# Kernel tuning notes

Hardware: AMD Instinct MI355X
Metric: run time of the kernel (lower is better)

The kernel has to match this reference:

```python
import jax, jax.numpy as jnp
import numpy as np

B, S, HID = 1, 2048, 4096
NH, NKV, D = 32, 8, 128          # query heads, kv heads, head_dim
GROUPS = NH // NKV               # GQA repeat factor = 4
WINDOW = 1024                    # sliding-window size
ROPE_BASE = 10000.0


def setup_inputs() -> dict:
    key = jax.random.key(0)
    k = jax.random.split(key, 5)
    hidden_states = jax.random.normal(k[0], (B, S, HID), jnp.float32)
    Wq = jax.random.normal(k[1], (HID, HID), jnp.float32) * 0.02
    Wk = jax.random.normal(k[2], (NKV * D, HID), jnp.float32) * 0.02
    Wv = jax.random.normal(k[3], (NKV * D, HID), jnp.float32) * 0.02
    Wo = jax.random.normal(k[4], (HID, HID), jnp.float32) * 0.02
    position_ids = jnp.arange(S, dtype=jnp.int64 if jax.config.jax_enable_x64 else jnp.int32)[None, :]
    # Sliding-window causal additive mask [B,1,S,S]: key j visible to query i iff i-WINDOW < j <= i
    i = jnp.arange(S)
    visible = (i[None, :] <= i[:, None]) & (i[:, None] - i[None, :] < WINDOW)
    neg = jnp.finfo(jnp.float32).min
    attention_mask = jnp.where(visible, 0.0, neg)[None, None, :, :].astype(jnp.float32)
    return {"hidden_states": hidden_states, "attention_mask": attention_mask,
            "position_ids": position_ids, "Wq": Wq, "Wk": Wk, "Wv": Wv, "Wo": Wo}


def _rotate_half(x):
    x1, x2 = x[..., : D // 2], x[..., D // 2:]
    return jnp.concatenate((-x2, x1), axis=-1)


def _rope_cos_sin(position_ids, dtype):
    # inv_freq over even dims; gather-by-position_ids == direct indexing
    inv_freq = 1.0 / (ROPE_BASE ** (jnp.arange(0, D, 2, dtype=jnp.float32) / D))  # [D/2]
    freqs = position_ids.astype(jnp.float32)[..., None] * inv_freq                # [B,S,D/2]
    emb = jnp.concatenate((freqs, freqs), axis=-1)                                # [B,S,D]
    cos = jnp.cos(emb)[:, None, :, :].astype(dtype)                               # [B,1,S,D]
    sin = jnp.sin(emb)[:, None, :, :].astype(dtype)
    return cos, sin


def reference(hidden_states, attention_mask, position_ids, Wq, Wk, Wv, Wo):
    bsz, q_len, _ = hidden_states.shape
    # projections (nn.Linear: y = x @ W.T)
    q = (hidden_states @ Wq.T).reshape(bsz, q_len, NH, D).transpose(0, 2, 1, 3)    # [B,NH,S,D]
    k = (hidden_states @ Wk.T).reshape(bsz, q_len, NKV, D).transpose(0, 2, 1, 3)   # [B,NKV,S,D]
    v = (hidden_states @ Wv.T).reshape(bsz, q_len, NKV, D).transpose(0, 2, 1, 3)
    cos, sin = _rope_cos_sin(position_ids, q.dtype)
    q = q * cos + _rotate_half(q) * sin
    k = k * cos + _rotate_half(k) * sin
    # GQA repeat_kv (repeat_interleave along head dim)
    k = jnp.repeat(k, GROUPS, axis=1)                                              # [B,NH,S,D]
    v = jnp.repeat(v, GROUPS, axis=1)
    scores = jnp.einsum('bhqd,bhkd->bhqk', q, k) / np.sqrt(D)                       # [B,NH,S,S]
    scores = scores + attention_mask
    scores = jnp.maximum(scores, jnp.finfo(scores.dtype).min)
    probs = jax.nn.softmax(scores.astype(jnp.float32), axis=-1).astype(q.dtype)
    out = jnp.einsum('bhqk,bhkd->bhqd', probs, v)                                   # [B,NH,S,D]
    out = out.transpose(0, 2, 1, 3).reshape(bsz, q_len, HID)
    return out @ Wo.T
```

## Files before the change

kernel.cpp:

```cpp
#include <hip/hip_runtime.h>

#define S_LEN 2048
#define HID   4096
#define NH    32
#define NKV   8
#define DH    128
#define KVD   (NKV*DH)
#define WIN   1024
#define NTOT  6144

typedef __bf16 bf16_t;
typedef __bf16 bfrag  __attribute__((ext_vector_type(8)));
typedef __bf16 bf4    __attribute__((ext_vector_type(4)));
typedef float  ffrag  __attribute__((ext_vector_type(4)));
typedef float  facc   __attribute__((ext_vector_type(16)));

__global__ __launch_bounds__(256) void cvt4_kernel(const float* __restrict__ h,
    const float* __restrict__ Wq, const float* __restrict__ Wk, const float* __restrict__ Wv,
    bf16_t* __restrict__ hB, bf16_t* __restrict__ WqB,
    bf16_t* __restrict__ WkB, bf16_t* __restrict__ WvB) {
  int i = blockIdx.x * 256 + threadIdx.x;
  const int N0 = S_LEN * HID / 4;
  const int N1 = N0 + HID * HID / 4;
  const int N2 = N1 + KVD * HID / 4;
  const float* s; bf16_t* d; int off;
  if (i < N0)      { s = h;  d = hB;  off = i; }
  else if (i < N1) { s = Wq; d = WqB; off = i - N0; }
  else if (i < N2) { s = Wk; d = WkB; off = i - N1; }
  else             { s = Wv; d = WvB; off = i - N2; }
  ffrag v = *(const ffrag*)(s + (size_t)off * 4);
  bf4 o;
  o[0] = (bf16_t)v[0]; o[1] = (bf16_t)v[1]; o[2] = (bf16_t)v[2]; o[3] = (bf16_t)v[3];
  *(bf4*)(d + (size_t)off * 4) = o;
}

__global__ __launch_bounds__(256) void rope_table_kernel(float2* __restrict__ tab) {
  int i = blockIdx.x * 256 + threadIdx.x;
  int s = i >> 6, d = i & 63;
  float inv = exp2f((float)d * (-13.287712379549449f / 64.f));
  float ang = (float)s * inv;
  tab[i] = make_float2(cosf(ang), sinf(ang));
}

__device__ __forceinline__ void load_lds16(const bf16_t* g, bf16_t* l) {
  __builtin_amdgcn_global_load_lds((__attribute__((address_space(1))) void*)g,
                                   (__attribute__((address_space(3))) void*)l,
                                   16, 0, 0);
}

#define BARW() asm volatile("s_barrier" ::: "memory")
#define WAITV(n) asm volatile("s_waitcnt vmcnt(" #n ")" ::: "memory")
#define LGKM0() do { asm volatile("s_waitcnt lgkmcnt(0)" ::: "memory"); \
                     __builtin_amdgcn_sched_barrier(0); } while (0)

__device__ __forceinline__ bfrag cvt8(const float4& a, const float4& b) {
  bfrag w;
  w[0] = (bf16_t)a.x; w[1] = (bf16_t)a.y; w[2] = (bf16_t)a.z; w[3] = (bf16_t)a.w;
  w[4] = (bf16_t)b.x; w[5] = (bf16_t)b.y; w[6] = (bf16_t)b.z; w[7] = (bf16_t)b.w;
  return w;
}

__global__ __launch_bounds__(512, 4) void gemm_qkv_kernel(const bf16_t* __restrict__ hB,
                                                          const bf16_t* __restrict__ Wqkv,
                                                          bf16_t* __restrict__ C) {
  constexpr int K     = 4096;
  constexpr int NT    = K / 64;
  constexpr int ABUFE = 128 * 64;
  constexpr int BBUFE = 192 * 64;
  __shared__ __align__(16) bf16_t lds[2 * ABUFE + 2 * BBUFE];
  bf16_t* As0 = lds;
  bf16_t* Bs0 = lds + 2 * ABUFE;

  const int raw  = blockIdx.x;
  const int xcd  = raw & 7;
  const int slot = raw >> 3;
  const int bx   = xcd * 4 + (slot & 3);
  const int by   = slot >> 2;
  const int row0 = by * 128;
  const int col0 = bx * 192;

  const int tid  = threadIdx.x;
  const int wave = tid >> 6;
  const int lane = tid & 63;
  const int wr = wave >> 2, wc = wave & 3;
  const int n = lane & 15, qd = lane >> 4;

  const int rsub = tid >> 3;
  const int sg   = (tid & 7) ^ (rsub & 7);
  const bf16_t* Ag = hB   + (size_t)(row0 + rsub) * K + sg * 8;
  const bf16_t* Bg = Wqkv + (size_t)(col0 + rsub) * K + sg * 8;
  const int wbase = wave * 512;

  const int pg0 = ( qd      ^ (n & 7)) * 8;
  const int pg1 = ((4 | qd) ^ (n & 7)) * 8;
  const int abase = (wr * 64 + n) * 64;
  const int bbase = (wc * 48 + n) * 64;

  ffrag acc[4][3];
#pragma unroll
  for (int mt = 0; mt < 4; ++mt)
#pragma unroll
    for (int nt = 0; nt < 3; ++nt) {
      acc[mt][nt][0] = 0.f; acc[mt][nt][1] = 0.f; acc[mt][nt][2] = 0.f; acc[mt][nt][3] = 0.f;
    }

  auto STAGE = [&](int t, int s) {
    const int ko = t * 64;
    bf16_t* as = As0 + s * ABUFE + wbase;
    bf16_t* bs = Bs0 + s * BBUFE + wbase;
    load_lds16(Ag + ko, as);
    load_lds16(Ag + (size_t)64 * K + ko, as + 4096);
    load_lds16(Bg + ko, bs);
    load_lds16(Bg + (size_t)64 * K + ko, bs + 4096);
    load_lds16(Bg + (size_t)128 * K + ko, bs + 8192);
  };

  STAGE(0, 0); STAGE(1, 1);
  WAITV(5);
  BARW();

  for (int t = 0; t < NT; ++t) {
    const int s = t & 1;
    const bf16_t* Asl = As0 + s * ABUFE;
    const bf16_t* Bsl = Bs0 + s * BBUFE;
    bfrag av[4], bv[3];

#pragma unroll
    for (int mt = 0; mt < 4; ++mt) av[mt] = *(const bfrag*)(Asl + abase + mt * 1024 + pg0);
#pragma unroll
    for (int nt = 0; nt < 3; ++nt) bv[nt] = *(const bfrag*)(Bsl + bbase + nt * 1024 + pg0);
    __builtin_amdgcn_s_setprio(1);
#pragma unroll
    for (int mt = 0; mt < 4; ++mt)
#pragma unroll
      for (int nt = 0; nt < 3; ++nt)
        acc[mt][nt] = __builtin_amdgcn_mfma_f32_16x16x32_bf16(av[mt], bv[nt], acc[mt][nt], 0, 0, 0);
    __builtin_amdgcn_s_setprio(0);

#pragma unroll
    for (int mt = 0; mt < 4; ++mt) av[mt] = *(const bfrag*)(Asl + abase + mt * 1024 + pg1);
#pragma unroll
    for (int nt = 0; nt < 3; ++nt) bv[nt] = *(const bfrag*)(Bsl + bbase + nt * 1024 + pg1);
    __builtin_amdgcn_s_setprio(1);
#pragma unroll
    for (int mt = 0; mt < 4; ++mt)
#pragma unroll
      for (int nt = 0; nt < 3; ++nt)
        acc[mt][nt] = __builtin_amdgcn_mfma_f32_16x16x32_bf16(av[mt], bv[nt], acc[mt][nt], 0, 0, 0);
    __builtin_amdgcn_s_setprio(0);

    LGKM0();
    BARW();
    if (t + 2 < NT) STAGE(t + 2, s);
    if (t + 1 < NT) {
      if (t + 2 < NT) { WAITV(5); } else { WAITV(0); }
      BARW();
    }
  }

  const int orow = row0 + wr * 64 + qd * 4;
  const int ocol = col0 + wc * 48 + n;
#pragma unroll
  for (int mt = 0; mt < 4; ++mt)
#pragma unroll
    for (int nt = 0; nt < 3; ++nt)
#pragma unroll
      for (int r = 0; r < 4; ++r)
        C[(size_t)(orow + mt * 16 + r) * NTOT + (ocol + nt * 16)] = (bf16_t)acc[mt][nt][r];
}

__global__ __launch_bounds__(256, 2) void gemm_out_kernel(const bf16_t* __restrict__ A,
                                                          const float* __restrict__ Wo,
                                                          float* __restrict__ out) {
  constexpr int K     = 4096;
  constexpr int NT    = K / 64;
  constexpr int ABUFE = 128 * 64;
  constexpr int BBUFE = 128 * 64;
  __shared__ __align__(16) bf16_t lds[2 * ABUFE + 2 * BBUFE];
  bf16_t* As0 = lds;
  bf16_t* Bs0 = lds + 2 * ABUFE;

  const int raw  = blockIdx.x;
  const int xcd  = raw & 7;
  const int slot = raw >> 3;
  const int bx   = xcd * 4 + (slot & 3);
  const int by   = slot >> 2;
  const int row0 = by * 128;
  const int col0 = bx * 128;

  const int tid  = threadIdx.x;
  const int wave = tid >> 6;
  const int lane = tid & 63;
  const int wm = wave >> 1, wn = wave & 1;
  const int l31 = lane & 31, hi = lane >> 5, l7 = lane & 7;

  const int rsub = tid >> 3;
  const int gA   = (tid & 7) ^ (rsub & 7);
  const bf16_t* Ag = A + (size_t)(row0 + rsub) * K + gA * 8;
  const int wbase = wave * 512;

  const int gB = tid & 7;
  const float* Bgf = Wo + (size_t)(col0 + rsub) * K;
  const int bwoff = rsub * 64 + ((gB ^ (rsub & 7)) * 8);

  int pgk[4];
#pragma unroll
  for (int ks = 0; ks < 4; ++ks) pgk[ks] = ((ks * 2 + hi) ^ l7) * 8;
  const int aoff = (wm * 64 + l31) * 64;
  const int boff = (wn * 64 + l31) * 64;

  facc acc[2][2];
#pragma unroll
  for (int mt = 0; mt < 2; ++mt)
#pragma unroll
    for (int nt = 0; nt < 2; ++nt)
#pragma unroll
      for (int j = 0; j < 16; ++j) acc[mt][nt][j] = 0.f;

  float4 bb00, bb01, bb10, bb11, bb20, bb21, bb30, bb31;

#define OUT_LOADB(t) do { const int ko_ = (t) * 64 + gB * 8;                        \
    bb00 = *(const float4*)(Bgf + ko_);                                             \
    bb01 = *(const float4*)(Bgf + ko_ + 4);                                         \
    bb10 = *(const float4*)(Bgf + (size_t)32 * K + ko_);                            \
    bb11 = *(const float4*)(Bgf + (size_t)32 * K + ko_ + 4);                        \
    bb20 = *(const float4*)(Bgf + (size_t)64 * K + ko_);                            \
    bb21 = *(const float4*)(Bgf + (size_t)64 * K + ko_ + 4);                        \
    bb30 = *(const float4*)(Bgf + (size_t)96 * K + ko_);                            \
    bb31 = *(const float4*)(Bgf + (size_t)96 * K + ko_ + 4); } while (0)
#define OUT_WRITEB(s) do { bf16_t* bs_ = Bs0 + (s) * BBUFE;                         \
    *(bfrag*)&bs_[bwoff]        = cvt8(bb00, bb01);                                 \
    *(bfrag*)&bs_[2048 + bwoff] = cvt8(bb10, bb11);                                 \
    *(bfrag*)&bs_[4096 + bwoff] = cvt8(bb20, bb21);                                 \
    *(bfrag*)&bs_[6144 + bwoff] = cvt8(bb30, bb31); } while (0)

  auto STAGE_A = [&](int t, int s) {
    const int ko = t * 64;
    bf16_t* as = As0 + s * ABUFE + wbase;
#pragma unroll
    for (int i = 0; i < 4; ++i)
      load_lds16(Ag + (size_t)(i * 32) * K + ko, as + i * 2048);
  };

  STAGE_A(0, 0); OUT_LOADB(0);
  WAITV(0);
  OUT_WRITEB(0);
  STAGE_A(1, 1); OUT_LOADB(1);
  LGKM0();
  BARW();

  for (int t = 0; t < NT; ++t) {
    const int s = t & 1;
    const bf16_t* Asl = As0 + s * ABUFE;
    const bf16_t* Bsl = Bs0 + s * BBUFE;

#pragma unroll
    for (int ks = 0; ks < 4; ++ks) {
      bfrag av0 = *(const bfrag*)(Asl + aoff + pgk[ks]);
      bfrag av1 = *(const bfrag*)(Asl + aoff + 2048 + pgk[ks]);
      bfrag bv0 = *(const bfrag*)(Bsl + boff + pgk[ks]);
      bfrag bv1 = *(const bfrag*)(Bsl + boff + 2048 + pgk[ks]);
      __builtin_amdgcn_s_setprio(1);
      acc[0][0] = __builtin_amdgcn_mfma_f32_32x32x16_bf16(av0, bv0, acc[0][0], 0, 0, 0);
      acc[0][1] = __builtin_amdgcn_mfma_f32_32x32x16_bf16(av0, bv1, acc[0][1], 0, 0, 0);
      acc[1][0] = __builtin_amdgcn_mfma_f32_32x32x16_bf16(av1, bv0, acc[1][0], 0, 0, 0);
      acc[1][1] = __builtin_amdgcn_mfma_f32_32x32x16_bf16(av1, bv1, acc[1][1], 0, 0, 0);
      __builtin_amdgcn_s_setprio(0);
    }

    LGKM0();
    BARW();
    if (t + 2 < NT) STAGE_A(t + 2, s);
    if (t + 1 < NT) {
      if (t + 2 < NT) { WAITV(4); } else { WAITV(0); }
      OUT_WRITEB(s ^ 1);
      if (t + 2 < NT) OUT_LOADB(t + 2);
      LGKM0();
      BARW();
    }
  }

  const int orow = row0 + wm * 64 + 4 * hi;
  const int ocol = col0 + wn * 64 + l31;
#pragma unroll
  for (int mt = 0; mt < 2; ++mt)
#pragma unroll
    for (int nt = 0; nt < 2; ++nt)
#pragma unroll
      for (int j = 0; j < 16; ++j) {
        int r = orow + mt * 32 + (j & 3) + 8 * (j >> 2);
        out[(size_t)r * HID + (ocol + nt * 32)] = acc[mt][nt][j];
      }
#undef OUT_LOADB
#undef OUT_WRITEB
}

__global__ __launch_bounds__(256) void ropecvt_kernel(const bf16_t* __restrict__ Cqkv,
                                                      const float2* __restrict__ tab,
                                                      bf16_t* __restrict__ Qb,
                                                      bf16_t* __restrict__ Kb,
                                                      bf16_t* __restrict__ Vb) {
  int idx = blockIdx.x * 256 + threadIdx.x;
  int g  = idx & 7;
  int t  = idx >> 3;
  int hh = t % 48;
  int s  = t / 48;
  const bf16_t* r0 = Cqkv + (size_t)s * NTOT + hh * 128;
  bfrag a0 = *(const bfrag*)&r0[g * 8];
  bfrag a1 = *(const bfrag*)&r0[g * 8 + 64];
  bf16_t* p;
  bool rope;
  if (hh < NH)           { p = Qb + (size_t)s * HID + hh * DH;        rope = true; }
  else if (hh < NH+NKV)  { p = Kb + (size_t)s * KVD + (hh - NH) * DH; rope = true; }
  else                   { p = Vb + (size_t)s * KVD + (hh - 40) * DH; rope = false; }
  bfrag o1, o2;
  if (rope) {
    const float2* tb = tab + s * 64 + g * 8;
#pragma unroll
    for (int j = 0; j < 8; ++j) {
      float x1 = (float)a0[j];
      float x2 = (float)a1[j];
      float2 cs = tb[j];
      o1[j] = (bf16_t)(x1 * cs.x - x2 * cs.y);
      o2[j] = (bf16_t)(x2 * cs.x + x1 * cs.y);
    }
  } else {
#pragma unroll
    for (int j = 0; j < 8; ++j) { o1[j] = a0[j]; o2[j] = a1[j]; }
  }
  *(bfrag*)&p[g * 8]      = o1;
  *(bfrag*)&p[g * 8 + 64] = o2;
}

#define KS_STRIDE 136
#define VT_STRIDE 72
#define PS_STRIDE 72

__global__ __launch_bounds__(256, 3) void attn_kernel(const bf16_t* __restrict__ Q,
                                                      const bf16_t* __restrict__ Kc,
                                                      const bf16_t* __restrict__ Vc,
                                                      bf16_t* __restrict__ AO) {
  const int qt   = 31 - blockIdx.x;
  const int h    = blockIdx.y;
  const int kvh  = h >> 2;
  const int q0   = qt * 64;
  const int tid  = threadIdx.x;
  const int wq   = tid >> 6;
  const int lane = tid & 63;
  const int n    = lane & 15;
  const int quad = lane >> 4;
  const float scale = 0.08838834764831845f;

  __shared__ __align__(16) bf16_t Ks[64 * KS_STRIDE];
  __shared__ __align__(16) bf16_t VT[128 * VT_STRIDE];
  __shared__ __align__(16) bf16_t Ps[4][16 * PS_STRIDE];

  bfrag aq[4];
#pragma unroll
  for (int kc = 0; kc < 4; ++kc) {
    bfrag t = *(const bfrag*)&Q[(size_t)(q0 + wq * 16 + n) * HID + h * DH + kc * 32 + quad * 8];
#pragma unroll
    for (int e = 0; e < 8; ++e) t[e] = (bf16_t)((float)t[e] * scale);
    aq[kc] = t;
  }

  ffrag acc[8];
#pragma unroll
  for (int dt = 0; dt < 8; ++dt) { acc[dt][0] = 0.f; acc[dt][1] = 0.f; acc[dt][2] = 0.f; acc[dt][3] = 0.f; }
  float lrow[4] = {0.f, 0.f, 0.f, 0.f};

  const int ktlo = (q0 >= WIN) ? ((q0 - (WIN - 1)) >> 6) : 0;
  const int kthi = (q0 + 63) >> 6;

  const int kg = tid & 15;
  const int dg = tid >> 4;

  bfrag pk[4], pv[4];
  {
    const int k0 = ktlo * 64;
#pragma unroll
    for (int i = 0; i < 4; ++i) {
      int pos = i * 256 + tid;
      pk[i] = *(const bfrag*)&Kc[(size_t)(k0 + (pos >> 4)) * KVD + kvh * DH + (pos & 15) * 8];
    }
#pragma unroll
    for (int j = 0; j < 4; ++j)
      pv[j] = *(const bfrag*)&Vc[(size_t)(k0 + j * 16 + kg) * KVD + kvh * DH + dg * 8];
  }

  for (int kt = ktlo; kt <= kthi; ++kt) {
    const int k0 = kt * 64;
    __syncthreads();
#pragma unroll
    for (int i = 0; i < 4; ++i) {
      int pos = i * 256 + tid;
      *(bfrag*)&Ks[(pos >> 4) * KS_STRIDE + (pos & 15) * 8] = pk[i];
    }
#pragma unroll
    for (int i = 0; i < 8; ++i) {
      bf4 pkk;
      pkk[0] = pv[0][i]; pkk[1] = pv[1][i]; pkk[2] = pv[2][i]; pkk[3] = pv[3][i];
      *(bf4*)&VT[(dg * 8 + i) * VT_STRIDE + kg * 4] = pkk;
    }
    __syncthreads();
    if (kt < kthi) {
      const int k1 = k0 + 64;
#pragma unroll
      for (int i = 0; i < 4; ++i) {
        int pos = i * 256 + tid;
        pk[i] = *(const bfrag*)&Kc[(size_t)(k1 + (pos >> 4)) * KVD + kvh * DH + (pos & 15) * 8];
      }
#pragma unroll
      for (int j = 0; j < 4; ++j)
        pv[j] = *(const bfrag*)&Vc[(size_t)(k1 + j * 16 + kg) * KVD + kvh * DH + dg * 8];
    }

    ffrag s[4];
#pragma unroll
    for (int nt = 0; nt < 4; ++nt) { s[nt][0] = 0.f; s[nt][1] = 0.f; s[nt][2] = 0.f; s[nt][3] = 0.f; }
#pragma unroll
    for (int kc = 0; kc < 4; ++kc) {
      bfrag bk[4];
#pragma unroll
      for (int nt = 0; nt < 4; ++nt)
        bk[nt] = *(const bfrag*)&Ks[(nt * 16 + n) * KS_STRIDE + kc * 32 + quad * 8];
      __builtin_amdgcn_s_setprio(1);
#pragma unroll
      for (int nt = 0; nt < 4; ++nt)
        s[nt] = __builtin_amdgcn_mfma_f32_16x16x32_bf16(aq[kc], bk[nt], s[nt], 0, 0, 0);
      __builtin_amdgcn_s_setprio(0);
    }

    const bool full = (k0 + 63 <= q0) && (q0 + 63 - k0 < WIN);
    if (!full) {
#pragma unroll
      for (int nt = 0; nt < 4; ++nt)
#pragma unroll
        for (int r = 0; r < 4; ++r) {
          int q = q0 + wq * 16 + quad * 4 + r;
          int k = k0 + nt * 16 + n;
          bool vis = (k <= q) && ((q - k) < WIN);
          if (!vis) s[nt][r] = -1e30f;
        }
    }

#pragma unroll
    for (int r = 0; r < 4; ++r) {
      bf4 pkk;
      float ps0 = __expf(s[0][r]);
      float ps1 = __expf(s[1][r]);
      float ps2 = __expf(s[2][r]);
      float ps3 = __expf(s[3][r]);
      lrow[r] += (ps0 + ps1) + (ps2 + ps3);
      pkk[0] = (bf16_t)ps0; pkk[1] = (bf16_t)ps1; pkk[2] = (bf16_t)ps2; pkk[3] = (bf16_t)ps3;
      *(bf4*)&Ps[wq][(quad * 4 + r) * PS_STRIDE + n * 4] = pkk;
    }

#pragma unroll
    for (int kc = 0; kc < 2; ++kc) {
      bfrag ap = *(const bfrag*)&Ps[wq][n * PS_STRIDE + kc * 32 + quad * 8];
#pragma unroll
      for (int dt = 0; dt < 8; dt += 4) {
        bfrag bv0 = *(const bfrag*)&VT[((dt + 0) * 16 + n) * VT_STRIDE + kc * 32 + quad * 8];
        bfrag bv1 = *(const bfrag*)&VT[((dt + 1) * 16 + n) * VT_STRIDE + kc * 32 + quad * 8];
        bfrag bv2 = *(const bfrag*)&VT[((dt + 2) * 16 + n) * VT_STRIDE + kc * 32 + quad * 8];
        bfrag bv3 = *(const bfrag*)&VT[((dt + 3) * 16 + n) * VT_STRIDE + kc * 32 + quad * 8];
        __builtin_amdgcn_s_setprio(1);
        acc[dt + 0] = __builtin_amdgcn_mfma_f32_16x16x32_bf16(ap, bv0, acc[dt + 0], 0, 0, 0);
        acc[dt + 1] = __builtin_amdgcn_mfma_f32_16x16x32_bf16(ap, bv1, acc[dt + 1], 0, 0, 0);
        acc[dt + 2] = __builtin_amdgcn_mfma_f32_16x16x32_bf16(ap, bv2, acc[dt + 2], 0, 0, 0);
        acc[dt + 3] = __builtin_amdgcn_mfma_f32_16x16x32_bf16(ap, bv3, acc[dt + 3], 0, 0, 0);
        __builtin_amdgcn_s_setprio(0);
      }
    }
  }

#pragma unroll
  for (int off = 1; off < 16; off <<= 1)
#pragma unroll
    for (int r = 0; r < 4; ++r) lrow[r] += __shfl_xor(lrow[r], off);
  float inv[4];
#pragma unroll
  for (int r = 0; r < 4; ++r) inv[r] = 1.f / lrow[r];
#pragma unroll
  for (int dt = 0; dt < 8; ++dt)
#pragma unroll
    for (int r = 0; r < 4; ++r)
      AO[(size_t)(q0 + wq * 16 + quad * 4 + r) * HID + h * DH + dt * 16 + n] =
          (bf16_t)(acc[dt][r] * inv[r]);
}

extern "C" void kernel_launch(void* const* d_in, const int* in_sizes, int n_in,
                              void* d_out, int out_size, void* d_ws, size_t ws_size,
                              hipStream_t stream) {
  const float* h  = (const float*)d_in[0];
  const float* Wq = (const float*)d_in[3];
  const float* Wk = (const float*)d_in[4];
  const float* Wv = (const float*)d_in[5];
  const float* Wo = (const float*)d_in[6];
  float* out = (float*)d_out;

  char* ws = (char*)d_ws;
  const size_t MB = (size_t)1 << 20;
  bf16_t* hB    = (bf16_t*)(ws + 0 * MB);
  bf16_t* Qb    = (bf16_t*)(ws + 0 * MB);
  bf16_t* WqB   = (bf16_t*)(ws + 16 * MB);
  bf16_t* WkB   = (bf16_t*)(ws + 48 * MB);
  bf16_t* WvB   = (bf16_t*)(ws + 56 * MB);
  bf16_t* Cqkv  = (bf16_t*)(ws + 64 * MB);
  float2* Rtab  = (float2*)(ws + 88 * MB);
  bf16_t* AOb   = (bf16_t*)(ws + 96 * MB);
  bf16_t* Kb    = (bf16_t*)(ws + 112 * MB);
  bf16_t* Vb    = (bf16_t*)(ws + 116 * MB);

  rope_table_kernel<<<(S_LEN * 64) / 256, 256, 0, stream>>>(Rtab);

  cvt4_kernel<<<(S_LEN * HID + HID * HID + 2 * KVD * HID) / 4 / 256, 256, 0, stream>>>(
      h, Wq, Wk, Wv, hB, WqB, WkB, WvB);

  gemm_qkv_kernel<<<512, 512, 0, stream>>>(hB, WqB, Cqkv);

  ropecvt_kernel<<<(S_LEN * 48 * 8) / 256, 256, 0, stream>>>(Cqkv, Rtab, Qb, Kb, Vb);

  attn_kernel<<<dim3(32, NH), 256, 0, stream>>>(Qb, Kb, Vb, AOb);

  gemm_out_kernel<<<512, 256, 0, stream>>>(AOb, Wo, out);
}
```

Baseline: 468.7 us.

## Fold Wo conversion into attention launch and rope table into cvt kernel

Moves the fp32-to-bf16 conversion of Wo out of gemm_out's inner loop into 64 extra blocks of the attention launch. This lets gemm_out stage both operands with direct global-to-LDS loads and drop the per-tile register conversion and extra LDS writes. Also merges the rope table computation into the cvt kernel to remove one launch. WoB reuses the Cqkv workspace region, which is assumed free by the time attention runs; the extra blocks share the attention launch and add memory traffic alongside the attention work.

```diff
diff --git a/kernel.cpp b/kernel.cpp
--- a/kernel.cpp
+++ b/kernel.cpp
@@ -18,11 +18,21 @@
 __global__ __launch_bounds__(256) void cvt4_kernel(const float* __restrict__ h,
     const float* __restrict__ Wq, const float* __restrict__ Wk, const float* __restrict__ Wv,
     bf16_t* __restrict__ hB, bf16_t* __restrict__ WqB,
-    bf16_t* __restrict__ WkB, bf16_t* __restrict__ WvB) {
+    bf16_t* __restrict__ WkB, bf16_t* __restrict__ WvB,
+    float2* __restrict__ tab) {
   int i = blockIdx.x * 256 + threadIdx.x;
   const int N0 = S_LEN * HID / 4;
   const int N1 = N0 + HID * HID / 4;
   const int N2 = N1 + KVD * HID / 4;
+  const int N3 = N2 + KVD * HID / 4;
+  if (i >= N3) {
+    int j = i - N3;
+    int s = j >> 6, d = j & 63;
+    float inv = exp2f((float)d * (-13.287712379549449f / 64.f));
+    float ang = (float)s * inv;
+    tab[j] = make_float2(cosf(ang), sinf(ang));
+    return;
+  }
   const float* s; bf16_t* d; int off;
   if (i < N0)      { s = h;  d = hB;  off = i; }
   else if (i < N1) { s = Wq; d = WqB; off = i - N0; }
@@ -34,14 +44,6 @@
   *(bf4*)(d + (size_t)off * 4) = o;
 }
 
-__global__ __launch_bounds__(256) void rope_table_kernel(float2* __restrict__ tab) {
-  int i = blockIdx.x * 256 + threadIdx.x;
-  int s = i >> 6, d = i & 63;
-  float inv = exp2f((float)d * (-13.287712379549449f / 64.f));
-  float ang = (float)s * inv;
-  tab[i] = make_float2(cosf(ang), sinf(ang));
-}
-
 __device__ __forceinline__ void load_lds16(const bf16_t* g, bf16_t* l) {
   __builtin_amdgcn_global_load_lds((__attribute__((address_space(1))) void*)g,
                                    (__attribute__((address_space(3))) void*)l,
@@ -52,13 +54,6 @@
 #define WAITV(n) asm volatile("s_waitcnt vmcnt(" #n ")" ::: "memory")
 #define LGKM0() do { asm volatile("s_waitcnt lgkmcnt(0)" ::: "memory"); \
                      __builtin_amdgcn_sched_barrier(0); } while (0)
-
-__device__ __forceinline__ bfrag cvt8(const float4& a, const float4& b) {
-  bfrag w;
-  w[0] = (bf16_t)a.x; w[1] = (bf16_t)a.y; w[2] = (bf16_t)a.z; w[3] = (bf16_t)a.w;
-  w[4] = (bf16_t)b.x; w[5] = (bf16_t)b.y; w[6] = (bf16_t)b.z; w[7] = (bf16_t)b.w;
-  return w;
-}
 
 __global__ __launch_bounds__(512, 4) void gemm_qkv_kernel(const bf16_t* __restrict__ hB,
                                                           const bf16_t* __restrict__ Wqkv,
@@ -170,7 +165,7 @@
 }
 
 __global__ __launch_bounds__(256, 2) void gemm_out_kernel(const bf16_t* __restrict__ A,
-                                                          const float* __restrict__ Wo,
+                                                          const bf16_t* __restrict__ B,
                                                           float* __restrict__ out) {
   constexpr int K     = 4096;
   constexpr int NT    = K / 64;
@@ -195,13 +190,10 @@
   const int l31 = lane & 31, hi = lane >> 5, l7 = lane & 7;
 
   const int rsub = tid >> 3;
-  const int gA   = (tid & 7) ^ (rsub & 7);
-  const bf16_t* Ag = A + (size_t)(row0 + rsub) * K + gA * 8;
+  const int sg   = (tid & 7) ^ (rsub & 7);
+  const bf16_t* Ag = A + (size_t)(row0 + rsub) * K + sg * 8;
+  const bf16_t* Bg = B + (size_t)(col0 + rsub) * K + sg * 8;
   const int wbase = wave * 512;
-
-  const int gB = tid & 7;
-  const float* Bgf = Wo + (size_t)(col0 + rsub) * K;
-  const int bwoff = rsub * 64 + ((gB ^ (rsub & 7)) * 8);
 
   int pgk[4];
 #pragma unroll
@@ -217,36 +209,19 @@
 #pragma unroll
       for (int j = 0; j < 16; ++j) acc[mt][nt][j] = 0.f;
 
-  float4 bb00, bb01, bb10, bb11, bb20, bb21, bb30, bb31;
-
-#define OUT_LOADB(t) do { const int ko_ = (t) * 64 + gB * 8;                        \
-    bb00 = *(const float4*)(Bgf + ko_);                                             \
-    bb01 = *(const float4*)(Bgf + ko_ + 4);                                         \
-    bb10 = *(const float4*)(Bgf + (size_t)32 * K + ko_);                            \
-    bb11 = *(const float4*)(Bgf + (size_t)32 * K + ko_ + 4);                        \
-    bb20 = *(const float4*)(Bgf + (size_t)64 * K + ko_);                            \
-    bb21 = *(const float4*)(Bgf + (size_t)64 * K + ko_ + 4);                        \
-    bb30 = *(const float4*)(Bgf + (size_t)96 * K + ko_);                            \
-    bb31 = *(const float4*)(Bgf + (size_t)96 * K + ko_ + 4); } while (0)
-#define OUT_WRITEB(s) do { bf16_t* bs_ = Bs0 + (s) * BBUFE;                         \
-    *(bfrag*)&bs_[bwoff]        = cvt8(bb00, bb01);                                 \
-    *(bfrag*)&bs_[2048 + bwoff] = cvt8(bb10, bb11);                                 \
-    *(bfrag*)&bs_[4096 + bwoff] = cvt8(bb20, bb21);                                 \
-    *(bfrag*)&bs_[6144 + bwoff] = cvt8(bb30, bb31); } while (0)
-
-  auto STAGE_A = [&](int t, int s) {
+  auto STAGE = [&](int t, int s) {
     const int ko = t * 64;
     bf16_t* as = As0 + s * ABUFE + wbase;
-#pragma unroll
-    for (int i = 0; i < 4; ++i)
+    bf16_t* bs = Bs0 + s * BBUFE + wbase;
+#pragma unroll
+    for (int i = 0; i < 4; ++i) {
       load_lds16(Ag + (size_t)(i * 32) * K + ko, as + i * 2048);
+      load_lds16(Bg + (size_t)(i * 32) * K + ko, bs + i * 2048);
+    }
   };
 
-  STAGE_A(0, 0); OUT_LOADB(0);
-  WAITV(0);
-  OUT_WRITEB(0);
-  STAGE_A(1, 1); OUT_LOADB(1);
-  LGKM0();
+  STAGE(0, 0); STAGE(1, 1);
+  WAITV(8);
   BARW();
 
   for (int t = 0; t < NT; ++t) {
@@ -270,12 +245,9 @@
 
     LGKM0();
     BARW();
-    if (t + 2 < NT) STAGE_A(t + 2, s);
+    if (t + 2 < NT) STAGE(t + 2, s);
     if (t + 1 < NT) {
-      if (t + 2 < NT) { WAITV(4); } else { WAITV(0); }
-      OUT_WRITEB(s ^ 1);
-      if (t + 2 < NT) OUT_LOADB(t + 2);
-      LGKM0();
+      if (t + 2 < NT) { WAITV(8); } else { WAITV(0); }
       BARW();
     }
   }
@@ -291,8 +263,6 @@
         int r = orow + mt * 32 + (j & 3) + 8 * (j >> 2);
         out[(size_t)r * HID + (ocol + nt * 32)] = acc[mt][nt][j];
       }
-#undef OUT_LOADB
-#undef OUT_WRITEB
 }
 
 __global__ __launch_bounds__(256) void ropecvt_kernel(const bf16_t* __restrict__ Cqkv,
@@ -339,12 +309,28 @@
 __global__ __launch_bounds__(256, 3) void attn_kernel(const bf16_t* __restrict__ Q,
                                                       const bf16_t* __restrict__ Kc,
                                                       const bf16_t* __restrict__ Vc,
-                                                      bf16_t* __restrict__ AO) {
+                                                      bf16_t* __restrict__ AO,
+                                                      const float* __restrict__ WoF,
+                                                      bf16_t* __restrict__ WoB) {
+  const int h    = blockIdx.y;
+  const int tid  = threadIdx.x;
+
+  if (h >= NH) {
+    const int NTH = 64 * 256;
+    int t0 = ((h - NH) * 32 + blockIdx.x) * 256 + tid;
+    for (int j = 0; j < (HID * HID / 4) / NTH; ++j) {
+      int i = t0 + j * NTH;
+      ffrag v = *(const ffrag*)(WoF + (size_t)i * 4);
+      bf4 o;
+      o[0] = (bf16_t)v[0]; o[1] = (bf16_t)v[1]; o[2] = (bf16_t)v[2]; o[3] = (bf16_t)v[3];
+      *(bf4*)(WoB + (size_t)i * 4) = o;
+    }
+    return;
+  }
+
   const int qt   = 31 - blockIdx.x;
-  const int h    = blockIdx.y;
   const int kvh  = h >> 2;
   const int q0   = qt * 64;
-  const int tid  = threadIdx.x;
   const int wq   = tid >> 6;
   const int lane = tid & 63;
   const int n    = lane & 15;
@@ -509,20 +495,19 @@
   bf16_t* WvB   = (bf16_t*)(ws + 56 * MB);
   bf16_t* Cqkv  = (bf16_t*)(ws + 64 * MB);
   float2* Rtab  = (float2*)(ws + 88 * MB);
+  bf16_t* WoB   = (bf16_t*)(ws + 64 * MB);
   bf16_t* AOb   = (bf16_t*)(ws + 96 * MB);
   bf16_t* Kb    = (bf16_t*)(ws + 112 * MB);
   bf16_t* Vb    = (bf16_t*)(ws + 116 * MB);
 
-  rope_table_kernel<<<(S_LEN * 64) / 256, 256, 0, stream>>>(Rtab);
-
-  cvt4_kernel<<<(S_LEN * HID + HID * HID + 2 * KVD * HID) / 4 / 256, 256, 0, stream>>>(
-      h, Wq, Wk, Wv, hB, WqB, WkB, WvB);
+  cvt4_kernel<<<(S_LEN * HID + HID * HID + 2 * KVD * HID + 4 * S_LEN * 64) / 4 / 256, 256, 0, stream>>>(
+      h, Wq, Wk, Wv, hB, WqB, WkB, WvB, Rtab);
 
   gemm_qkv_kernel<<<512, 512, 0, stream>>>(hB, WqB, Cqkv);
 
   ropecvt_kernel<<<(S_LEN * 48 * 8) / 256, 256, 0, stream>>>(Cqkv, Rtab, Qb, Kb, Vb);
 
-  attn_kernel<<<dim3(32, NH), 256, 0, stream>>>(Qb, Kb, Vb, AOb);
-
-  gemm_out_kernel<<<512, 256, 0, stream>>>(AOb, Wo, out);
-}
+  attn_kernel<<<dim3(32, NH + 2), 256, 0, stream>>>(Qb, Kb, Vb, AOb, Wo, WoB);
+
+  gemm_out_kernel<<<512, 256, 0, stream>>>(AOb, WoB, out);
+}
```

Measured after the change: 452.9 us (median of 2 runs). 3.4% less time.
